# Kernel optimization log

Hardware: AMD Instinct MI355X
Metric: run time of the kernel (lower is better)

Reference implementation:

```python
import jax, jax.numpy as jnp
import numpy as np

EPS = 1e-9
SPREAD_WEIGHT = 0.1
QUAD_WEIGHT = 1.0

N_NODES = 200000
N_EDGES = 12800000
DIM = 128


def to_uhg_space(x):
    # dim > 2: truncate to first 2 features, append homogeneous 1 -> [..., 3]
    ones = jnp.ones((*x.shape[:-1], 1), dtype=x.dtype)
    return jnp.concatenate([x[..., :2], ones], axis=-1)


def uhg_inner(a, b):
    # -<spatial,spatial> + time*time, keepdim
    return -jnp.sum(a[..., :-1] * b[..., :-1], axis=-1, keepdims=True) + a[..., -1:] * b[..., -1:]


def uhg_quadrance(a, b):
    aa = uhg_inner(a, a)
    bb = uhg_inner(b, b)
    ab = uhg_inner(a, b)
    num = ab * ab - aa * bb
    den = aa * bb
    safe = jnp.maximum(jnp.abs(den), EPS) * jnp.sign(den)
    return (num / safe).squeeze(-1)


# spread has the identical formula, applied to lines instead of points
uhg_spread = uhg_quadrance


def setup_inputs() -> dict:
    key = jax.random.key(0)
    k1, k2 = jax.random.split(key)
    z = jax.random.normal(k1, (N_NODES, DIM), dtype=jnp.float32)
    edge_index = jax.random.randint(k2, (2, N_EDGES), 0, N_NODES, dtype=jnp.int32)
    return {"z": z, "edge_index": edge_index}


def reference(z, edge_index):
    z_uhg = to_uhg_space(z)                      # [N, 3]
    src, dst = edge_index[0], edge_index[1]
    # proximity: quadrance over all edges (gather + fused elementwise + mean)
    quad = uhg_quadrance(z_uhg[src], z_uhg[dst])  # [E]
    proximity_loss = quad.mean()
    # compactness: quadrance of every node to the origin [0,0,1]
    origin = jnp.zeros((1, 3), dtype=z.dtype).at[:, -1].set(1.0)
    compactness_loss = uhg_quadrance(z_uhg, origin).mean()
    # lines: vectorized cross product of each point with the origin
    lines = jnp.cross(z_uhg, origin)              # [N, 3]
    # spread over the first min(10, E) edges only (as in the original)
    n_sp = min(10, edge_index.shape[1])
    sp = uhg_spread(lines[src[:n_sp]], lines[dst[:n_sp]])
    spread_loss = sp.mean()
    loss = QUAD_WEIGHT * (proximity_loss + compactness_loss) + SPREAD_WEIGHT * spread_loss
    return loss
```

## Files before the change

### kernel.cpp

```cpp
#include <hip/hip_runtime.h>
#include <hip/hip_bf16.h>

#define UHG_EPS 1e-9
#define ZDIM 128

#define EDGE_BLOCKS 1024
#define NODE_BLOCKS 1024
#define BLOCK 256

#define PART_SHIFT 13
#define PART_SIZE (1 << PART_SHIFT)
#define P_MAX 25
#define NBINS_MAX (P_MAX * P_MAX)
#define STAGE_CAP 28
#define CHUNK 16
#define SCAT_BLOCKS 512
#define SBLOCK 512
#define EPB 4
#define BBLOCK 1024
#define SENTINEL 0xFFFFFFFFu
#define OVGUARD 4096u
#define GPAD 16

#define PROX_OFF 0
#define COMP_OFF (16 * 1024)
#define GCUR_OFF (24 * 1024)
#define TABLE_OFF (128 * 1024)

typedef float vfloat2 __attribute__((ext_vector_type(2)));
typedef int vint4 __attribute__((ext_vector_type(4)));
typedef unsigned uvec4 __attribute__((ext_vector_type(4)));

__device__ vfloat2 llvm_amdgcn_raw_buffer_load_v2f32(vint4 rsrc, int voffset, int soffset,
                                                     int cpol) __asm("llvm.amdgcn.raw.buffer.load.v2f32");

__device__ __forceinline__ vint4 make_srd(const void* base, unsigned int bytes) {
    union { const void* p; unsigned int w[2]; } pb;
    pb.p = base;
    vint4 r;
    r.x = (int)pb.w[0];
    r.y = (int)pb.w[1];
    r.z = (int)bytes;
    r.w = 0x00020000;
    return r;
}


__device__ __forceinline__ double safe_den(double den) {
    return copysign(fmax(fabs(den), UHG_EPS), den);
}

__device__ __forceinline__ double quad_xy(vfloat2 a, vfloat2 b) {
    double xa = a.x, ya = a.y, xb = b.x, yb = b.y;
    double aa = 1.0 - (xa * xa + ya * ya);
    double bb = 1.0 - (xb * xb + yb * yb);
    double ab = 1.0 - (xa * xb + ya * yb);
    double den = aa * bb;
    double num = ab * ab - den;
    return num / safe_den(den);
}

__device__ __forceinline__ double block_reduce(double v, double* sh) {
    int lane = threadIdx.x & 63;
    int wid = threadIdx.x >> 6;
    v += __shfl_down(v, 32);
    v += __shfl_down(v, 16);
    v += __shfl_down(v, 8);
    v += __shfl_down(v, 4);
    v += __shfl_down(v, 2);
    v += __shfl_down(v, 1);
    if (lane == 0) sh[wid] = v;
    __syncthreads();
    double r = 0.0;
    if (wid == 0) {
        int nw = (int)(blockDim.x >> 6);
        r = (lane < nw) ? sh[lane] : 0.0;
        r += __shfl_down(r, 8);
        r += __shfl_down(r, 4);
        r += __shfl_down(r, 2);
        r += __shfl_down(r, 1);
    }
    __syncthreads();
    return r;
}


__global__ __launch_bounds__(BLOCK) void node_kernel(const float* __restrict__ z,
                                                     vfloat2* __restrict__ table,
                                                     double* __restrict__ comp_partials, int N,
                                                     unsigned* __restrict__ gcur, int nbins) {
    __shared__ double sh[16];
    if (gcur && blockIdx.x == 0) {
        for (int j = threadIdx.x; j < 2 * nbins * GPAD; j += BLOCK) gcur[j] = 0u;
    }
    const vfloat2* zp = (const vfloat2*)z;
    double local = 0.0;
    for (int i = blockIdx.x * BLOCK + threadIdx.x; i < N; i += NODE_BLOCKS * BLOCK) {
        vfloat2 v = zp[(size_t)i * (ZDIM / 2)];
        if (table) table[i] = v;
        double x = v.x, y = v.y;
        double aa = 1.0 - (x * x + y * y);
        local += (1.0 - aa) / safe_den(aa);
    }
    double tot = block_reduce(local, sh);
    if (threadIdx.x == 0) comp_partials[blockIdx.x] = tot;
}

__global__ __launch_bounds__(SBLOCK) void scatter_kernel(const int* __restrict__ src,
                                                         const int* __restrict__ dst, int E,
                                                         int P, int nbins,
                                                         unsigned* __restrict__ gcur,
                                                         unsigned* __restrict__ gbins,
                                                         int bincap) {
    __shared__ unsigned cnt[NBINS_MAX];
    __shared__ __align__(16) unsigned stage[NBINS_MAX][STAGE_CAP];
    const int tid = threadIdx.x;

    for (int b = tid; b < nbins; b += SBLOCK) cnt[b] = 0u;
    __syncthreads();

#define OVFLOW(B, V)                                                                      \
    {                                                                                     \
        unsigned _hp = atomicAdd(&gcur[(size_t)(nbins + (B)) * GPAD], 1u);                \
        if (_hp < OVGUARD) gbins[(size_t)(B) * bincap + (bincap - 1 - (int)_hp)] = (V);   \
    }

    auto flush_bins = [&](bool final_pad) {
        for (int b = tid; b < nbins; b += SBLOCK) {
            unsigned n = cnt[b];
            unsigned m = n < (unsigned)STAGE_CAP ? n : (unsigned)STAGE_CAP;
            while (m >= (unsigned)CHUNK) {
                unsigned pos = atomicAdd(&gcur[(size_t)b * GPAD], (unsigned)CHUNK);
                if (pos + CHUNK <= (unsigned)bincap) {
                    unsigned* out = gbins + (size_t)b * bincap + pos;
#pragma unroll
                    for (int j = 0; j < CHUNK / 4; ++j)
                        *(uvec4*)(out + 4 * j) = *(const uvec4*)&stage[b][4 * j];
                } else {
                    for (int j = 0; j < CHUNK; ++j) OVFLOW(b, stage[b][j]);
                }
                for (unsigned j = CHUNK; j < m; ++j) stage[b][j - CHUNK] = stage[b][j];
                m -= CHUNK;
            }
            if (final_pad && m > 0) {
                for (unsigned j = m; j < (unsigned)CHUNK; ++j) stage[b][j] = SENTINEL;
                unsigned pos = atomicAdd(&gcur[(size_t)b * GPAD], (unsigned)CHUNK);
                if (pos + CHUNK <= (unsigned)bincap) {
                    unsigned* out = gbins + (size_t)b * bincap + pos;
#pragma unroll
                    for (int j = 0; j < CHUNK / 4; ++j)
                        *(uvec4*)(out + 4 * j) = *(const uvec4*)&stage[b][4 * j];
                } else {
                    for (unsigned j = 0; j < m; ++j) OVFLOW(b, stage[b][j]);
                }
                m = 0;
            }
            cnt[b] = m;
        }
    };

    long e0 = ((long)blockIdx.x * E / SCAT_BLOCKS) & ~3L;
    long e1 = (blockIdx.x == SCAT_BLOCKS - 1)
                  ? (long)E
                  : (((long)(blockIdx.x + 1) * E / SCAT_BLOCKS) & ~3L);
    long span = e1 - e0;
    long nbatch = span / (EPB * SBLOCK);
    long rem0 = e0 + nbatch * EPB * SBLOCK;

    const vint4* s4 = (const vint4*)(src + e0);
    const vint4* d4 = (const vint4*)(dst + e0);

    vint4 cs = {}, cd = {};
    if (nbatch > 0) {
        cs = __builtin_nontemporal_load(s4 + tid);
        cd = __builtin_nontemporal_load(d4 + tid);
    }
    for (long k = 0; k < nbatch; ++k) {
        vint4 s = cs, d = cd;
        if (k + 1 < nbatch) {
            cs = __builtin_nontemporal_load(s4 + (k + 1) * SBLOCK + tid);
            cd = __builtin_nontemporal_load(d4 + (k + 1) * SBLOCK + tid);
        }
        __builtin_amdgcn_sched_barrier(0);
        int bn0 = (s.x >> PART_SHIFT) * P + (d.x >> PART_SHIFT);
        int bn1 = (s.y >> PART_SHIFT) * P + (d.y >> PART_SHIFT);
        int bn2 = (s.z >> PART_SHIFT) * P + (d.z >> PART_SHIFT);
        int bn3 = (s.w >> PART_SHIFT) * P + (d.w >> PART_SHIFT);
        unsigned vl0 = (unsigned)(s.x & (PART_SIZE - 1)) | ((unsigned)(d.x & (PART_SIZE - 1)) << PART_SHIFT);
        unsigned vl1 = (unsigned)(s.y & (PART_SIZE - 1)) | ((unsigned)(d.y & (PART_SIZE - 1)) << PART_SHIFT);
        unsigned vl2 = (unsigned)(s.z & (PART_SIZE - 1)) | ((unsigned)(d.z & (PART_SIZE - 1)) << PART_SHIFT);
        unsigned vl3 = (unsigned)(s.w & (PART_SIZE - 1)) | ((unsigned)(d.w & (PART_SIZE - 1)) << PART_SHIFT);
        unsigned sl0 = atomicAdd(&cnt[bn0], 1u);
        unsigned sl1 = atomicAdd(&cnt[bn1], 1u);
        unsigned sl2 = atomicAdd(&cnt[bn2], 1u);
        unsigned sl3 = atomicAdd(&cnt[bn3], 1u);
        if (sl0 < (unsigned)STAGE_CAP) stage[bn0][sl0] = vl0; else OVFLOW(bn0, vl0);
        if (sl1 < (unsigned)STAGE_CAP) stage[bn1][sl1] = vl1; else OVFLOW(bn1, vl1);
        if (sl2 < (unsigned)STAGE_CAP) stage[bn2][sl2] = vl2; else OVFLOW(bn2, vl2);
        if (sl3 < (unsigned)STAGE_CAP) stage[bn3][sl3] = vl3; else OVFLOW(bn3, vl3);
        __syncthreads();
        flush_bins(false);
        __syncthreads();
    }
    for (long i = rem0 + tid; i < e1; i += SBLOCK) {
        int s = src[i], d = dst[i];
        int bn = (s >> PART_SHIFT) * P + (d >> PART_SHIFT);
        unsigned vl = (unsigned)(s & (PART_SIZE - 1)) | ((unsigned)(d & (PART_SIZE - 1)) << PART_SHIFT);
        unsigned sl = atomicAdd(&cnt[bn], 1u);
        if (sl < (unsigned)STAGE_CAP) stage[bn][sl] = vl; else OVFLOW(bn, vl);
    }
    __syncthreads();
    flush_bins(true);
#undef OVFLOW
}

__global__ __launch_bounds__(BBLOCK) void binned_edge_kernel(const vfloat2* __restrict__ table,
                                                             int N, int P,
                                                             const unsigned* __restrict__ gcur,
                                                             const unsigned* __restrict__ gbins,
                                                             int bincap,
                                                             double* __restrict__ prox_partials) {
    __shared__ vfloat2 pts[2][PART_SIZE];
    __shared__ double sh[16];
    const int bin = blockIdx.x;
    const int sp = bin / P, dp = bin % P;
    const int tid = threadIdx.x;
    const int nbins = P * P;

    for (int j = tid; j < PART_SIZE; j += BBLOCK) {
        int gs = (sp << PART_SHIFT) + j;
        int gd = (dp << PART_SHIFT) + j;
        vfloat2 zv = {0.0f, 0.0f};
        pts[0][j] = (gs < N) ? table[gs] : zv;
        pts[1][j] = (gd < N) ? table[gd] : zv;
    }
    __syncthreads();

    unsigned lo = gcur[(size_t)bin * GPAD];
    if (lo > (unsigned)bincap) lo = (unsigned)bincap;
    unsigned hi = gcur[(size_t)(nbins + bin) * GPAD];
    if (hi > OVGUARD) hi = OVGUARD;
    const unsigned* eb = gbins + (size_t)bin * bincap;
    const uvec4* eb4 = (const uvec4*)eb;

    double local = 0.0;
    unsigned nv = lo >> 2;
    unsigned i = tid;
    bool have = i < nv;
    uvec4 cur = {};
    if (have) cur = __builtin_nontemporal_load(eb4 + i);
    while (have) {
        unsigned in2 = i + BBLOCK;
        bool hn = in2 < nv;
        uvec4 nxt = {};
        if (hn) nxt = __builtin_nontemporal_load(eb4 + in2);
        __builtin_amdgcn_sched_barrier(0);
        vfloat2 a0 = pts[0][cur.x & (PART_SIZE - 1u)], b0 = pts[1][(cur.x >> PART_SHIFT) & (PART_SIZE - 1u)];
        vfloat2 a1 = pts[0][cur.y & (PART_SIZE - 1u)], b1 = pts[1][(cur.y >> PART_SHIFT) & (PART_SIZE - 1u)];
        vfloat2 a2 = pts[0][cur.z & (PART_SIZE - 1u)], b2 = pts[1][(cur.z >> PART_SHIFT) & (PART_SIZE - 1u)];
        vfloat2 a3 = pts[0][cur.w & (PART_SIZE - 1u)], b3 = pts[1][(cur.w >> PART_SHIFT) & (PART_SIZE - 1u)];
        if (cur.x != SENTINEL) local += quad_xy(a0, b0);
        if (cur.y != SENTINEL) local += quad_xy(a1, b1);
        if (cur.z != SENTINEL) local += quad_xy(a2, b2);
        if (cur.w != SENTINEL) local += quad_xy(a3, b3);
        cur = nxt;
        i = in2;
        have = hn;
    }
    for (unsigned j = (nv << 2) + tid; j < lo; j += BBLOCK) {
        unsigned v = eb[j];
        if (v != SENTINEL)
            local += quad_xy(pts[0][v & (PART_SIZE - 1u)],
                             pts[1][(v >> PART_SHIFT) & (PART_SIZE - 1u)]);
    }
    for (unsigned j = tid; j < hi; j += BBLOCK) {
        unsigned v = eb[bincap - 1 - (int)j];
        local += quad_xy(pts[0][v & (PART_SIZE - 1u)],
                         pts[1][(v >> PART_SHIFT) & (PART_SIZE - 1u)]);
    }
    double tot = block_reduce(local, sh);
    if (tid == 0) prox_partials[bin] = tot;
}

#define GATHER8(dsta, i0, i1)                                                   \
    dsta[0] = llvm_amdgcn_raw_buffer_load_v2f32(srd, (i0).x << SHIFT, 0, 1);    \
    dsta[1] = llvm_amdgcn_raw_buffer_load_v2f32(srd, (i0).y << SHIFT, 0, 1);    \
    dsta[2] = llvm_amdgcn_raw_buffer_load_v2f32(srd, (i0).z << SHIFT, 0, 1);    \
    dsta[3] = llvm_amdgcn_raw_buffer_load_v2f32(srd, (i0).w << SHIFT, 0, 1);    \
    dsta[4] = llvm_amdgcn_raw_buffer_load_v2f32(srd, (i1).x << SHIFT, 0, 1);    \
    dsta[5] = llvm_amdgcn_raw_buffer_load_v2f32(srd, (i1).y << SHIFT, 0, 1);    \
    dsta[6] = llvm_amdgcn_raw_buffer_load_v2f32(srd, (i1).z << SHIFT, 0, 1);    \
    dsta[7] = llvm_amdgcn_raw_buffer_load_v2f32(srd, (i1).w << SHIFT, 0, 1);

template <int COMPACT>
__global__ __launch_bounds__(BLOCK) void edge_kernel(const vint4* __restrict__ src4,
                                                     const vint4* __restrict__ dst4, int nvec,
                                                     const int* __restrict__ src,
                                                     const int* __restrict__ dst, int E,
                                                     const void* __restrict__ xy, int N,
                                                     double* __restrict__ prox_partials) {
    __shared__ double sh[16];
    double local = 0.0;
    int tid = blockIdx.x * BLOCK + threadIdx.x;
    const int gstride = EDGE_BLOCKS * BLOCK;
    const int SHIFT = COMPACT ? 3 : 9;

    vint4 srd = make_srd(xy, COMPACT ? (unsigned int)N * 8u : (unsigned int)N * 512u);

    int nvec2 = nvec / 2;
    int v0 = tid;
    bool p0 = v0 < nvec2;
    int v1 = v0 + gstride;
    bool p1 = v1 < nvec2;

    vint4 is0 = {}, is1 = {}, id0 = {}, id1 = {};
    vfloat2 ca[8] = {}, cb[8] = {};
    vfloat2 na[8] = {}, nb[8] = {};

    if (p0) {
        vint4 s0 = __builtin_nontemporal_load(src4 + 2 * (long)v0);
        vint4 s1 = __builtin_nontemporal_load(src4 + 2 * (long)v0 + 1);
        vint4 d0 = __builtin_nontemporal_load(dst4 + 2 * (long)v0);
        vint4 d1 = __builtin_nontemporal_load(dst4 + 2 * (long)v0 + 1);
        GATHER8(ca, s0, s1);
        GATHER8(cb, d0, d1);
    }
    if (p1) {
        is0 = __builtin_nontemporal_load(src4 + 2 * (long)v1);
        is1 = __builtin_nontemporal_load(src4 + 2 * (long)v1 + 1);
        id0 = __builtin_nontemporal_load(dst4 + 2 * (long)v1);
        id1 = __builtin_nontemporal_load(dst4 + 2 * (long)v1 + 1);
    }

    while (p0) {
        if (p1) {
            GATHER8(na, is0, is1);
            GATHER8(nb, id0, id1);
        }
        int v2 = v1 + gstride;
        bool p2 = v2 < nvec2;
        if (p2) {
            is0 = __builtin_nontemporal_load(src4 + 2 * (long)v2);
            is1 = __builtin_nontemporal_load(src4 + 2 * (long)v2 + 1);
            id0 = __builtin_nontemporal_load(dst4 + 2 * (long)v2);
            id1 = __builtin_nontemporal_load(dst4 + 2 * (long)v2 + 1);
        }
        __builtin_amdgcn_sched_barrier(0);
#pragma unroll
        for (int i = 0; i < 8; ++i) local += quad_xy(ca[i], cb[i]);
#pragma unroll
        for (int i = 0; i < 8; ++i) { ca[i] = na[i]; cb[i] = nb[i]; }
        p0 = p1;
        v1 = v2;
        p1 = p2;
    }

    for (int e = 8 * nvec2 + tid; e < E; e += gstride) {
        vfloat2 a = llvm_amdgcn_raw_buffer_load_v2f32(srd, src[e] << SHIFT, 0, 1);
        vfloat2 b = llvm_amdgcn_raw_buffer_load_v2f32(srd, dst[e] << SHIFT, 0, 1);
        local += quad_xy(a, b);
    }
    double tot = block_reduce(local, sh);
    if (threadIdx.x == 0) prox_partials[blockIdx.x] = tot;
}

__global__ __launch_bounds__(BLOCK) void finalize_kernel(const int* __restrict__ src,
                                                         const int* __restrict__ dst,
                                                         const float* __restrict__ z,
                                                         const double* __restrict__ prox_partials,
                                                         int nprox,
                                                         const double* __restrict__ comp_partials,
                                                         float* __restrict__ out, int N, int E) {
    __shared__ double sh[16];
    int t = threadIdx.x;

    double pl = 0.0;
    for (int i = t; i < nprox; i += BLOCK) pl += prox_partials[i];
    double prox = block_reduce(pl, sh);

    double cl = 0.0;
    for (int i = t; i < NODE_BLOCKS; i += BLOCK) cl += comp_partials[i];
    double comp = block_reduce(cl, sh);

    int n_sp = E < 10 ? E : 10;
    double sl = 0.0;
    if (t < n_sp) {
        int s = src[t], d = dst[t];
        double xa = z[(size_t)s * ZDIM], ya = z[(size_t)s * ZDIM + 1];
        double xb = z[(size_t)d * ZDIM], yb = z[(size_t)d * ZDIM + 1];
        double aa = -(ya * ya + xa * xa);
        double bb = -(yb * yb + xb * xb);
        double ab = -(ya * yb + xa * xb);
        double den = aa * bb;
        sl = (ab * ab - den) / safe_den(den);
    }
    double spread = block_reduce(sl, sh);

    if (t == 0) {
        double loss = prox / (double)E + comp / (double)N;
        if (n_sp > 0) loss += 0.1 * (spread / (double)n_sp);
        out[0] = (float)loss;
    }
}


extern "C" void kernel_launch(void* const* d_in, const int* in_sizes, int n_in,
                              void* d_out, int out_size, void* d_ws, size_t ws_size,
                              hipStream_t stream) {
    const float* z = (const float*)d_in[0];
    const int* edge_index = (const int*)d_in[1];
    float* out = (float*)d_out;

    const int N = in_sizes[0] / ZDIM;
    const int E = in_sizes[1] / 2;
    const int* src = edge_index;
    const int* dst = edge_index + (size_t)E;

    double* prox_partials = (double*)((char*)d_ws + PROX_OFF);
    double* comp_partials = (double*)((char*)d_ws + COMP_OFF);
    unsigned* gcur = (unsigned*)((char*)d_ws + GCUR_OFF);
    vfloat2* table = (vfloat2*)((char*)d_ws + TABLE_OFF);
    bool use_table = ws_size >= TABLE_OFF + (size_t)N * sizeof(vfloat2);

    const int P = (N + PART_SIZE - 1) >> PART_SHIFT;
    const int nbins = P * P;
    size_t gbins_off = TABLE_OFF + (((size_t)N * 8 + 255) & ~(size_t)255);
    bool use_binned = false;
    unsigned* gbins = nullptr;
    int bincap = 0;
    if (use_table && P >= 1 && P <= P_MAX && nbins <= NBINS_MAX && E > nbins * 64 &&
        ws_size > gbins_off) {
        int mean = E / nbins;
        int cap_want = (mean + 5504) & ~31;
        int need_min = mean + 5208;
        size_t avail = ws_size - gbins_off;
        int cap_fit = (int)((avail / ((size_t)nbins * 4)) & ~(size_t)31);
        bincap = cap_fit < cap_want ? cap_fit : cap_want;
        if (bincap >= need_min) {
            use_binned = true;
            gbins = (unsigned*)((char*)d_ws + gbins_off);
        }
    }

    node_kernel<<<NODE_BLOCKS, BLOCK, 0, stream>>>(z, use_table ? table : nullptr,
                                                   comp_partials,
                                                   N, use_binned ? gcur : nullptr, nbins);

    if (use_binned) {
        scatter_kernel<<<SCAT_BLOCKS, SBLOCK, 0, stream>>>(src, dst, E, P, nbins, gcur, gbins,
                                                           bincap);
        binned_edge_kernel<<<nbins, BBLOCK, 0, stream>>>(table, N, P, gcur, gbins, bincap,
                                                         prox_partials);
        finalize_kernel<<<1, BLOCK, 0, stream>>>(src, dst, z, prox_partials, nbins,
                                                 comp_partials, out, N, E);
    } else {
        int nvec = E / 4;
        if (use_table) {
            edge_kernel<1><<<EDGE_BLOCKS, BLOCK, 0, stream>>>((const vint4*)src,
                                                              (const vint4*)dst, nvec, src, dst,
                                                              E, table, N, prox_partials);
        } else {
            edge_kernel<0><<<EDGE_BLOCKS, BLOCK, 0, stream>>>((const vint4*)src,
                                                              (const vint4*)dst, nvec, src, dst,
                                                              E, z, N, prox_partials);
        }
        finalize_kernel<<<1, BLOCK, 0, stream>>>(src, dst, z, prox_partials, EDGE_BLOCKS,
                                                 comp_partials, out, N, E);
    }
}
```

Baseline: 286.4 us.

## Use per-wave staging in scatter, fuse node pass, split bins across two blocks

Replaces the block-wide staging in the edge-binning scatter kernel with a small per-wave staging area that flushes groups of four entries, so the two __syncthreads per batch go away. The node/compactness pass and table build move into the scatter kernel, and the counters are cleared with hipMemsetAsync instead. The binned edge kernel launches two blocks per bin, each covering half of the bin's entries, to increase parallelism. In exchange it issues many more global atomics because each flush moves only four entries, scans every bin each iteration, and needs more LDS per block for the wave-private staging.

```diff
diff --git a/kernel.cpp b/kernel.cpp
--- a/kernel.cpp
+++ b/kernel.cpp
@@ -12,19 +12,18 @@
 #define PART_SIZE (1 << PART_SHIFT)
 #define P_MAX 25
 #define NBINS_MAX (P_MAX * P_MAX)
-#define STAGE_CAP 28
-#define CHUNK 16
-#define SCAT_BLOCKS 512
+#define SCAT_BLOCKS 256
 #define SBLOCK 512
-#define EPB 4
+#define NWAVES (SBLOCK / 64)
+#define SDEPTH 4
 #define BBLOCK 1024
 #define SENTINEL 0xFFFFFFFFu
-#define OVGUARD 4096u
+#define OVGUARD 1024
 #define GPAD 16
 
 #define PROX_OFF 0
 #define COMP_OFF (16 * 1024)
-#define GCUR_OFF (24 * 1024)
+#define GCUR_OFF (32 * 1024)
 #define TABLE_OFF (128 * 1024)
 
 typedef float vfloat2 __attribute__((ext_vector_type(2)));
@@ -60,15 +59,20 @@
     return num / safe_den(den);
 }
 
-__device__ __forceinline__ double block_reduce(double v, double* sh) {
-    int lane = threadIdx.x & 63;
-    int wid = threadIdx.x >> 6;
+__device__ __forceinline__ double wave_reduce(double v) {
     v += __shfl_down(v, 32);
     v += __shfl_down(v, 16);
     v += __shfl_down(v, 8);
     v += __shfl_down(v, 4);
     v += __shfl_down(v, 2);
     v += __shfl_down(v, 1);
+    return v;
+}
+
+__device__ __forceinline__ double block_reduce(double v, double* sh) {
+    int lane = threadIdx.x & 63;
+    int wid = threadIdx.x >> 6;
+    v = wave_reduce(v);
     if (lane == 0) sh[wid] = v;
     __syncthreads();
     double r = 0.0;
@@ -87,12 +91,8 @@
 
 __global__ __launch_bounds__(BLOCK) void node_kernel(const float* __restrict__ z,
                                                      vfloat2* __restrict__ table,
-                                                     double* __restrict__ comp_partials, int N,
-                                                     unsigned* __restrict__ gcur, int nbins) {
+                                                     double* __restrict__ comp_partials, int N) {
     __shared__ double sh[16];
-    if (gcur && blockIdx.x == 0) {
-        for (int j = threadIdx.x; j < 2 * nbins * GPAD; j += BLOCK) gcur[j] = 0u;
-    }
     const vfloat2* zp = (const vfloat2*)z;
     double local = 0.0;
     for (int i = blockIdx.x * BLOCK + threadIdx.x; i < N; i += NODE_BLOCKS * BLOCK) {
@@ -106,112 +106,141 @@
     if (threadIdx.x == 0) comp_partials[blockIdx.x] = tot;
 }
 
-__global__ __launch_bounds__(SBLOCK) void scatter_kernel(const int* __restrict__ src,
+__global__ __launch_bounds__(SBLOCK) void scatter_kernel(const float* __restrict__ z,
+                                                         vfloat2* __restrict__ table,
+                                                         double* __restrict__ comp_partials,
+                                                         int N,
+                                                         const int* __restrict__ src,
                                                          const int* __restrict__ dst, int E,
                                                          int P, int nbins,
                                                          unsigned* __restrict__ gcur,
                                                          unsigned* __restrict__ gbins,
                                                          int bincap) {
-    __shared__ unsigned cnt[NBINS_MAX];
-    __shared__ __align__(16) unsigned stage[NBINS_MAX][STAGE_CAP];
+    __shared__ unsigned cnt[NWAVES][NBINS_MAX];
+    __shared__ __align__(16) unsigned stage[NWAVES][NBINS_MAX][SDEPTH];
     const int tid = threadIdx.x;
-
-    for (int b = tid; b < nbins; b += SBLOCK) cnt[b] = 0u;
+    const int lane = tid & 63;
+    const int wid = tid >> 6;
+    const int TOTW = SCAT_BLOCKS * NWAVES;
+    const int gw = blockIdx.x * NWAVES + wid;
+    const unsigned botlim = (unsigned)(bincap - OVGUARD);
+
+    for (int b = tid; b < nbins; b += SBLOCK) {
+#pragma unroll
+        for (int w = 0; w < NWAVES; ++w) cnt[w][b] = 0u;
+    }
     __syncthreads();
 
-#define OVFLOW(B, V)                                                                      \
-    {                                                                                     \
-        unsigned _hp = atomicAdd(&gcur[(size_t)(nbins + (B)) * GPAD], 1u);                \
-        if (_hp < OVGUARD) gbins[(size_t)(B) * bincap + (bincap - 1 - (int)_hp)] = (V);   \
-    }
-
-    auto flush_bins = [&](bool final_pad) {
-        for (int b = tid; b < nbins; b += SBLOCK) {
-            unsigned n = cnt[b];
-            unsigned m = n < (unsigned)STAGE_CAP ? n : (unsigned)STAGE_CAP;
-            while (m >= (unsigned)CHUNK) {
-                unsigned pos = atomicAdd(&gcur[(size_t)b * GPAD], (unsigned)CHUNK);
-                if (pos + CHUNK <= (unsigned)bincap) {
-                    unsigned* out = gbins + (size_t)b * bincap + pos;
-#pragma unroll
-                    for (int j = 0; j < CHUNK / 4; ++j)
-                        *(uvec4*)(out + 4 * j) = *(const uvec4*)&stage[b][4 * j];
+    {
+        const vfloat2* zp = (const vfloat2*)z;
+        long n0 = (long)gw * N / TOTW, n1 = (long)(gw + 1) * N / TOTW;
+        double comp = 0.0;
+        for (long i = n0 + lane; i < n1; i += 64) {
+            vfloat2 v = zp[(size_t)i * (ZDIM / 2)];
+            table[i] = v;
+            double x = v.x, y = v.y;
+            double aa = 1.0 - (x * x + y * y);
+            comp += (1.0 - aa) / safe_den(aa);
+        }
+        comp = wave_reduce(comp);
+        if (lane == 0) comp_partials[gw] = comp;
+    }
+
+    auto ovf = [&](int b, unsigned v) {
+        unsigned hp = atomicAdd(&gcur[(size_t)(nbins + b) * GPAD], 1u);
+        if (hp < (unsigned)OVGUARD)
+            gbins[(size_t)b * bincap + (bincap - 1 - (int)hp)] = v;
+    };
+    auto insert = [&](int s, int d) {
+        int bn = (s >> PART_SHIFT) * P + (d >> PART_SHIFT);
+        unsigned vl = (unsigned)(s & (PART_SIZE - 1)) |
+                      ((unsigned)(d & (PART_SIZE - 1)) << PART_SHIFT);
+        unsigned slot = atomicAdd(&cnt[wid][bn], 1u);
+        if (slot < (unsigned)SDEPTH) stage[wid][bn][slot] = vl;
+        else ovf(bn, vl);
+    };
+    auto scan_flush = [&]() {
+        for (int b = lane; b < nbins; b += 64) {
+            if (cnt[wid][b] >= (unsigned)SDEPTH) {
+                uvec4 val = *(const uvec4*)&stage[wid][b][0];
+                unsigned pos = atomicAdd(&gcur[(size_t)b * GPAD], (unsigned)SDEPTH);
+                if (pos + SDEPTH <= botlim) {
+                    *(uvec4*)(gbins + (size_t)b * bincap + pos) = val;
                 } else {
-                    for (int j = 0; j < CHUNK; ++j) OVFLOW(b, stage[b][j]);
+                    ovf(b, val.x); ovf(b, val.y); ovf(b, val.z); ovf(b, val.w);
                 }
-                for (unsigned j = CHUNK; j < m; ++j) stage[b][j - CHUNK] = stage[b][j];
-                m -= CHUNK;
+                cnt[wid][b] = 0u;
             }
-            if (final_pad && m > 0) {
-                for (unsigned j = m; j < (unsigned)CHUNK; ++j) stage[b][j] = SENTINEL;
-                unsigned pos = atomicAdd(&gcur[(size_t)b * GPAD], (unsigned)CHUNK);
-                if (pos + CHUNK <= (unsigned)bincap) {
-                    unsigned* out = gbins + (size_t)b * bincap + pos;
-#pragma unroll
-                    for (int j = 0; j < CHUNK / 4; ++j)
-                        *(uvec4*)(out + 4 * j) = *(const uvec4*)&stage[b][4 * j];
-                } else {
-                    for (unsigned j = 0; j < m; ++j) OVFLOW(b, stage[b][j]);
+        }
+    };
+
+    const long nv4 = (long)E / 4;
+    long v0 = (long)gw * nv4 / TOTW, v1 = (long)(gw + 1) * nv4 / TOTW;
+    const vint4* s4 = (const vint4*)src;
+    const vint4* d4 = (const vint4*)dst;
+
+    long niter = (v1 - v0 + 63) >> 6;
+    long i = v0 + lane;
+    vint4 cs = {}, cd = {};
+    if (i < v1) {
+        cs = __builtin_nontemporal_load(s4 + i);
+        cd = __builtin_nontemporal_load(d4 + i);
+    }
+    for (long k = 0; k < niter; ++k) {
+        bool valid = i < v1;
+        vint4 s = cs, d = cd;
+        long inext = i + 64;
+        if (inext < v1) {
+            cs = __builtin_nontemporal_load(s4 + inext);
+            cd = __builtin_nontemporal_load(d4 + inext);
+        }
+        __builtin_amdgcn_sched_barrier(0);
+        if (valid) {
+            insert(s.x, d.x);
+            insert(s.y, d.y);
+            insert(s.z, d.z);
+            insert(s.w, d.w);
+        }
+        scan_flush();
+        i = inext;
+    }
+    if (gw == TOTW - 1) {
+        for (long e = 4 * nv4 + lane; e < E; e += 64) insert(src[e], dst[e]);
+        scan_flush();
+    }
+
+    __syncthreads();
+    for (int b = tid; b < nbins; b += SBLOCK) {
+        unsigned buf[SDEPTH];
+        int m = 0;
+        for (int w = 0; w < NWAVES; ++w) {
+            unsigned n = cnt[w][b];
+            if (n > (unsigned)SDEPTH) n = (unsigned)SDEPTH;
+            for (unsigned j = 0; j < n; ++j) {
+                buf[m++] = stage[w][b][j];
+                if (m == SDEPTH) {
+                    unsigned pos = atomicAdd(&gcur[(size_t)b * GPAD], (unsigned)SDEPTH);
+                    if (pos + SDEPTH <= botlim) {
+                        uvec4 v4v = {buf[0], buf[1], buf[2], buf[3]};
+                        *(uvec4*)(gbins + (size_t)b * bincap + pos) = v4v;
+                    } else {
+                        for (int j2 = 0; j2 < SDEPTH; ++j2) ovf(b, buf[j2]);
+                    }
+                    m = 0;
                 }
-                m = 0;
             }
-            cnt[b] = m;
-        }
-    };
-
-    long e0 = ((long)blockIdx.x * E / SCAT_BLOCKS) & ~3L;
-    long e1 = (blockIdx.x == SCAT_BLOCKS - 1)
-                  ? (long)E
-                  : (((long)(blockIdx.x + 1) * E / SCAT_BLOCKS) & ~3L);
-    long span = e1 - e0;
-    long nbatch = span / (EPB * SBLOCK);
-    long rem0 = e0 + nbatch * EPB * SBLOCK;
-
-    const vint4* s4 = (const vint4*)(src + e0);
-    const vint4* d4 = (const vint4*)(dst + e0);
-
-    vint4 cs = {}, cd = {};
-    if (nbatch > 0) {
-        cs = __builtin_nontemporal_load(s4 + tid);
-        cd = __builtin_nontemporal_load(d4 + tid);
-    }
-    for (long k = 0; k < nbatch; ++k) {
-        vint4 s = cs, d = cd;
-        if (k + 1 < nbatch) {
-            cs = __builtin_nontemporal_load(s4 + (k + 1) * SBLOCK + tid);
-            cd = __builtin_nontemporal_load(d4 + (k + 1) * SBLOCK + tid);
-        }
-        __builtin_amdgcn_sched_barrier(0);
-        int bn0 = (s.x >> PART_SHIFT) * P + (d.x >> PART_SHIFT);
-        int bn1 = (s.y >> PART_SHIFT) * P + (d.y >> PART_SHIFT);
-        int bn2 = (s.z >> PART_SHIFT) * P + (d.z >> PART_SHIFT);
-        int bn3 = (s.w >> PART_SHIFT) * P + (d.w >> PART_SHIFT);
-        unsigned vl0 = (unsigned)(s.x & (PART_SIZE - 1)) | ((unsigned)(d.x & (PART_SIZE - 1)) << PART_SHIFT);
-        unsigned vl1 = (unsigned)(s.y & (PART_SIZE - 1)) | ((unsigned)(d.y & (PART_SIZE - 1)) << PART_SHIFT);
-        unsigned vl2 = (unsigned)(s.z & (PART_SIZE - 1)) | ((unsigned)(d.z & (PART_SIZE - 1)) << PART_SHIFT);
-        unsigned vl3 = (unsigned)(s.w & (PART_SIZE - 1)) | ((unsigned)(d.w & (PART_SIZE - 1)) << PART_SHIFT);
-        unsigned sl0 = atomicAdd(&cnt[bn0], 1u);
-        unsigned sl1 = atomicAdd(&cnt[bn1], 1u);
-        unsigned sl2 = atomicAdd(&cnt[bn2], 1u);
-        unsigned sl3 = atomicAdd(&cnt[bn3], 1u);
-        if (sl0 < (unsigned)STAGE_CAP) stage[bn0][sl0] = vl0; else OVFLOW(bn0, vl0);
-        if (sl1 < (unsigned)STAGE_CAP) stage[bn1][sl1] = vl1; else OVFLOW(bn1, vl1);
-        if (sl2 < (unsigned)STAGE_CAP) stage[bn2][sl2] = vl2; else OVFLOW(bn2, vl2);
-        if (sl3 < (unsigned)STAGE_CAP) stage[bn3][sl3] = vl3; else OVFLOW(bn3, vl3);
-        __syncthreads();
-        flush_bins(false);
-        __syncthreads();
-    }
-    for (long i = rem0 + tid; i < e1; i += SBLOCK) {
-        int s = src[i], d = dst[i];
-        int bn = (s >> PART_SHIFT) * P + (d >> PART_SHIFT);
-        unsigned vl = (unsigned)(s & (PART_SIZE - 1)) | ((unsigned)(d & (PART_SIZE - 1)) << PART_SHIFT);
-        unsigned sl = atomicAdd(&cnt[bn], 1u);
-        if (sl < (unsigned)STAGE_CAP) stage[bn][sl] = vl; else OVFLOW(bn, vl);
-    }
-    __syncthreads();
-    flush_bins(true);
-#undef OVFLOW
+        }
+        if (m > 0) {
+            for (int j = m; j < SDEPTH; ++j) buf[j] = SENTINEL;
+            unsigned pos = atomicAdd(&gcur[(size_t)b * GPAD], (unsigned)SDEPTH);
+            if (pos + SDEPTH <= botlim) {
+                uvec4 v4v = {buf[0], buf[1], buf[2], buf[3]};
+                *(uvec4*)(gbins + (size_t)b * bincap + pos) = v4v;
+            } else {
+                for (int j2 = 0; j2 < m; ++j2) ovf(b, buf[j2]);
+            }
+        }
+    }
 }
 
 __global__ __launch_bounds__(BBLOCK) void binned_edge_kernel(const vfloat2* __restrict__ table,
@@ -222,10 +251,12 @@
                                                              double* __restrict__ prox_partials) {
     __shared__ vfloat2 pts[2][PART_SIZE];
     __shared__ double sh[16];
-    const int bin = blockIdx.x;
+    const int bin = blockIdx.x >> 1;
+    const int half = blockIdx.x & 1;
     const int sp = bin / P, dp = bin % P;
     const int tid = threadIdx.x;
     const int nbins = P * P;
+    const unsigned botlim = (unsigned)(bincap - OVGUARD);
 
     for (int j = tid; j < PART_SIZE; j += BBLOCK) {
         int gs = (sp << PART_SHIFT) + j;
@@ -237,21 +268,25 @@
     __syncthreads();
 
     unsigned lo = gcur[(size_t)bin * GPAD];
-    if (lo > (unsigned)bincap) lo = (unsigned)bincap;
+    if (lo > botlim) lo = botlim;
     unsigned hi = gcur[(size_t)(nbins + bin) * GPAD];
-    if (hi > OVGUARD) hi = OVGUARD;
+    if (hi > (unsigned)OVGUARD) hi = (unsigned)OVGUARD;
     const unsigned* eb = gbins + (size_t)bin * bincap;
-    const uvec4* eb4 = (const uvec4*)eb;
+
+    unsigned h0 = (lo >> 1) & ~3u;
+    unsigned rs = half ? h0 : 0u;
+    unsigned re = half ? lo : h0;
 
     double local = 0.0;
-    unsigned nv = lo >> 2;
+    unsigned ng = (re - rs) >> 2;
+    const uvec4* eb4 = (const uvec4*)(eb + rs);
     unsigned i = tid;
-    bool have = i < nv;
+    bool have = i < ng;
     uvec4 cur = {};
     if (have) cur = __builtin_nontemporal_load(eb4 + i);
     while (have) {
         unsigned in2 = i + BBLOCK;
-        bool hn = in2 < nv;
+        bool hn = in2 < ng;
         uvec4 nxt = {};
         if (hn) nxt = __builtin_nontemporal_load(eb4 + in2);
         __builtin_amdgcn_sched_barrier(0);
@@ -267,19 +302,21 @@
         i = in2;
         have = hn;
     }
-    for (unsigned j = (nv << 2) + tid; j < lo; j += BBLOCK) {
+    for (unsigned j = rs + (ng << 2) + tid; j < re; j += BBLOCK) {
         unsigned v = eb[j];
         if (v != SENTINEL)
             local += quad_xy(pts[0][v & (PART_SIZE - 1u)],
                              pts[1][(v >> PART_SHIFT) & (PART_SIZE - 1u)]);
     }
-    for (unsigned j = tid; j < hi; j += BBLOCK) {
-        unsigned v = eb[bincap - 1 - (int)j];
-        local += quad_xy(pts[0][v & (PART_SIZE - 1u)],
-                         pts[1][(v >> PART_SHIFT) & (PART_SIZE - 1u)]);
+    if (half) {
+        for (unsigned j = tid; j < hi; j += BBLOCK) {
+            unsigned v = eb[bincap - 1 - (int)j];
+            local += quad_xy(pts[0][v & (PART_SIZE - 1u)],
+                             pts[1][(v >> PART_SHIFT) & (PART_SIZE - 1u)]);
+        }
     }
     double tot = block_reduce(local, sh);
-    if (tid == 0) prox_partials[bin] = tot;
+    if (tid == 0) prox_partials[blockIdx.x] = tot;
 }
 
 #define GATHER8(dsta, i0, i1)                                                   \
@@ -370,6 +407,7 @@
                                                          const double* __restrict__ prox_partials,
                                                          int nprox,
                                                          const double* __restrict__ comp_partials,
+                                                         int ncomp,
                                                          float* __restrict__ out, int N, int E) {
     __shared__ double sh[16];
     int t = threadIdx.x;
@@ -379,7 +417,7 @@
     double prox = block_reduce(pl, sh);
 
     double cl = 0.0;
-    for (int i = t; i < NODE_BLOCKS; i += BLOCK) cl += comp_partials[i];
+    for (int i = t; i < ncomp; i += BLOCK) cl += comp_partials[i];
     double comp = block_reduce(cl, sh);
 
     int n_sp = E < 10 ? E : 10;
@@ -431,8 +469,8 @@
     if (use_table && P >= 1 && P <= P_MAX && nbins <= NBINS_MAX && E > nbins * 64 &&
         ws_size > gbins_off) {
         int mean = E / nbins;
-        int cap_want = (mean + 5504) & ~31;
-        int need_min = mean + 5208;
+        int cap_want = (mean + 768 + 2048 + OVGUARD + 31) & ~31;
+        int need_min = mean + 512 + 1024 + OVGUARD;
         size_t avail = ws_size - gbins_off;
         int cap_fit = (int)((avail / ((size_t)nbins * 4)) & ~(size_t)31);
         bincap = cap_fit < cap_want ? cap_fit : cap_want;
@@ -442,18 +480,19 @@
         }
     }
 
-    node_kernel<<<NODE_BLOCKS, BLOCK, 0, stream>>>(z, use_table ? table : nullptr,
-                                                   comp_partials,
-                                                   N, use_binned ? gcur : nullptr, nbins);
-
     if (use_binned) {
-        scatter_kernel<<<SCAT_BLOCKS, SBLOCK, 0, stream>>>(src, dst, E, P, nbins, gcur, gbins,
-                                                           bincap);
-        binned_edge_kernel<<<nbins, BBLOCK, 0, stream>>>(table, N, P, gcur, gbins, bincap,
-                                                         prox_partials);
-        finalize_kernel<<<1, BLOCK, 0, stream>>>(src, dst, z, prox_partials, nbins,
-                                                 comp_partials, out, N, E);
+        hipMemsetAsync(gcur, 0, (size_t)2 * nbins * GPAD * sizeof(unsigned), stream);
+        scatter_kernel<<<SCAT_BLOCKS, SBLOCK, 0, stream>>>(z, table, comp_partials, N,
+                                                           src, dst, E, P, nbins, gcur,
+                                                           gbins, bincap);
+        binned_edge_kernel<<<2 * nbins, BBLOCK, 0, stream>>>(table, N, P, gcur, gbins, bincap,
+                                                             prox_partials);
+        finalize_kernel<<<1, BLOCK, 0, stream>>>(src, dst, z, prox_partials, 2 * nbins,
+                                                 comp_partials, SCAT_BLOCKS * NWAVES,
+                                                 out, N, E);
     } else {
+        node_kernel<<<NODE_BLOCKS, BLOCK, 0, stream>>>(z, use_table ? table : nullptr,
+                                                       comp_partials, N);
         int nvec = E / 4;
         if (use_table) {
             edge_kernel<1><<<EDGE_BLOCKS, BLOCK, 0, stream>>>((const vint4*)src,
@@ -465,6 +504,6 @@
                                                               E, z, N, prox_partials);
         }
         finalize_kernel<<<1, BLOCK, 0, stream>>>(src, dst, z, prox_partials, EDGE_BLOCKS,
-                                                 comp_partials, out, N, E);
-    }
-}
+                                                 comp_partials, NODE_BLOCKS, out, N, E);
+    }
+}
```

Measured after the change: 467.1 us. 1.63x slower.
